# Performance work log

Measured on AMD Instinct MI355X. Metric: run time of the kernel, lower is better.

## Reference

```python
import jax, jax.numpy as jnp
import numpy as np

DIM = 64
HEADS = 4            # self.num_heads = 2 * num_heads(=2)
SMK = 5
KS = 7
EPS = 1e-5
SCALE = (DIM // HEADS) ** -0.5


def pool_mat(n, out=7):
    # AdaptiveAvgPool2d bin matrix: P[i, j] = 1/size if floor(i*n/out) <= j < ceil((i+1)*n/out)
    P = np.zeros((out, n), np.float32)
    for i in range(out):
        s = (i * n) // out
        e = -((-(i + 1) * n) // out)
        P[i, s:e] = 1.0 / (e - s)
    return jnp.asarray(P)


def bn(x, g, b, m, v):
    # inference BatchNorm2d on [B,C,H,W]
    return (x - m[:, None, None]) * (g[:, None, None] * jax.lax.rsqrt(v[:, None, None] + EPS)) + b[:, None, None]


def conv1x1(x, w):
    return jnp.einsum('oi,bihw->bohw', w, x)


def rpb_bias(rpb, H, W, k):
    # replicate apply_rpb gather indexing (incl. the flip over flattened HW)
    rs = 2 * k - 1
    ih0 = np.arange(k)
    idx_k = (ih0[:, None] * rs + ih0[None, :]).reshape(-1)        # [k*k]
    rh = np.ones(k, np.int64); rh[k // 2] = H - (k - 1)
    rw = np.ones(k, np.int64); rw[k // 2] = W - (k - 1)
    ih = np.repeat(ih0, rh)                                       # [H]
    iw = np.repeat(ih0, rw)                                       # [W]
    bias_hw = ih[:, None] * rs + iw[None, :]                      # [H,W]
    bias_idx = (bias_hw[..., None] + idx_k).reshape(-1, k * k)[::-1].copy()  # [H*W,k*k]
    flat = rpb.reshape(rpb.shape[0], -1)                          # [G, rs*rs]
    return flat[:, bias_idx].reshape(1, rpb.shape[0], H, W, k * k)


def na2d_av(attn, value, k):
    # NATTEN-style neighborhood AV: window start clamped to stay in-bounds
    B, G, H, W, _ = attn.shape
    si = np.clip(np.arange(H) - k // 2, 0, H - k)
    sj = np.clip(np.arange(W) - k // 2, 0, W - k)
    ii = si[:, None] + np.arange(k)    # [H,k]
    jj = sj[:, None] + np.arange(k)    # [W,k]
    v = value[:, :, ii][:, :, :, :, jj]         # [B,G,H,k,W,k,C]
    a = attn.reshape(B, G, H, W, k, k)
    return jnp.einsum('bghwij,bghiwjc->bghwc', a, v)


def reference(x, wq_w, wq_g, wq_b, wq_m, wq_v,
              wk_w, wk_g, wk_b, wk_m, wk_v,
              proj_w, proj_b, rpb1, rpb2,
              dy_w, dy_g, dy_b, dy_m, dy_v):
    B, C, H, W = x.shape
    G = HEADS
    q, kctx = jnp.split(x, 2, axis=1)                      # [B,C/2,H,W] each
    q = bn(conv1x1(q, wq_w), wq_g, wq_b, wq_m, wq_v) * SCALE
    Ph, Pw = pool_mat(H), pool_mat(W)
    kp = jnp.einsum('ph,bchw,qw->bcpq', Ph, kctx, Pw)      # adaptive avg pool to 7x7
    k = bn(conv1x1(kp, wk_w), wk_g, wk_b, wk_m, wk_v)
    q = q.reshape(B, G, -1, H * W)                          # b g c n
    k = k.reshape(B, G, -1, 49)                             # b g c l
    w = jnp.einsum('bgcn,bgcl->bgnl', q, k)
    w = w.transpose(0, 3, 1, 2)                             # b l g n
    w = jnp.einsum('ol,blgn->bogn', proj_w, w) + proj_b[None, :, None, None]  # b (74) g n
    w = w.transpose(0, 2, 3, 1).reshape(B, G, H, W, SMK * SMK + KS * KS)
    attn1 = w[..., :SMK * SMK]
    attn2 = w[..., SMK * SMK:]
    attn1 = jax.nn.softmax(attn1 + rpb_bias(rpb1, H, W, SMK), axis=-1)
    attn2 = jax.nn.softmax(attn2 + rpb_bias(rpb2, H, W, KS), axis=-1)
    c = C // (2 * G)
    value = x.reshape(B, 2, G, c, H, W).transpose(1, 0, 2, 4, 5, 3)  # m b g h w c
    x1 = na2d_av(attn1, value[0], SMK)
    x2 = na2d_av(attn2, value[1], KS)
    out = jnp.concatenate([x1, x2], axis=1)                 # b (2g) h w c
    out = out.transpose(0, 1, 4, 2, 3).reshape(B, C, H, W)  # b (g c) h w
    return bn(conv1x1(out, dy_w), dy_g, dy_b, dy_m, dy_v)


def setup_inputs() -> dict:
    key = jax.random.key(0)
    ks = jax.random.split(key, 20)
    h = DIM // 2
    def bnp(k):
        k1, k2, k3, k4 = jax.random.split(k, 4)
        return (jax.random.uniform(k1, (0,)),)  # unused
    inp = {
        'x': jax.random.normal(ks[0], (8, DIM, 64, 64), jnp.float32),
        'wq_w': jax.random.normal(ks[1], (h, h), jnp.float32) * (h ** -0.5),
        'wq_g': jax.random.uniform(ks[2], (h,), jnp.float32, 0.5, 1.5),
        'wq_b': jax.random.normal(ks[3], (h,), jnp.float32) * 0.1,
        'wq_m': jax.random.normal(ks[4], (h,), jnp.float32) * 0.1,
        'wq_v': jax.random.uniform(ks[5], (h,), jnp.float32, 0.5, 1.5),
        'wk_w': jax.random.normal(ks[6], (h, h), jnp.float32) * (h ** -0.5),
        'wk_g': jax.random.uniform(ks[7], (h,), jnp.float32, 0.5, 1.5),
        'wk_b': jax.random.normal(ks[8], (h,), jnp.float32) * 0.1,
        'wk_m': jax.random.normal(ks[9], (h,), jnp.float32) * 0.1,
        'wk_v': jax.random.uniform(ks[10], (h,), jnp.float32, 0.5, 1.5),
        'proj_w': jax.random.normal(ks[11], (SMK * SMK + KS * KS, 49), jnp.float32) * (49 ** -0.5),
        'proj_b': jax.random.normal(ks[12], (SMK * SMK + KS * KS,), jnp.float32) * 0.02,
        'rpb1': jax.random.normal(ks[13], (HEADS, 2 * SMK - 1, 2 * SMK - 1), jnp.float32) * 0.02,
        'rpb2': jax.random.normal(ks[14], (HEADS, 2 * KS - 1, 2 * KS - 1), jnp.float32) * 0.02,
        'dy_w': jax.random.normal(ks[15], (DIM, DIM), jnp.float32) * (DIM ** -0.5),
        'dy_g': jax.random.uniform(ks[16], (DIM,), jnp.float32, 0.5, 1.5),
        'dy_b': jax.random.normal(ks[17], (DIM,), jnp.float32) * 0.1,
        'dy_m': jax.random.normal(ks[18], (DIM,), jnp.float32) * 0.1,
        'dy_v': jax.random.uniform(ks[19], (DIM,), jnp.float32, 0.5, 1.5),
    }
    return inp
```

## Files before the change

### kernel.cpp

```cpp
#include <hip/hip_runtime.h>

#define EPSV 1e-5f

#define OFF_W    12544
#define OFF_WQT  31488
#define OFF_DYT  32512

typedef float f4u __attribute__((ext_vector_type(4), aligned(4)));

__global__ __launch_bounds__(512) void prep_weights(
    const float* __restrict__ wq_w, const float* __restrict__ dy_w,
    float* __restrict__ ws)
{
  const int t = blockIdx.x * 512 + threadIdx.x;
  float* wqT = ws + OFF_WQT;
  float* dyT = ws + OFF_DYT;
  if (t < 1024) {
    const int i = t >> 5, o = t & 31;
    wqT[t] = wq_w[o * 32 + i];
  }
  const int t2 = t - 1024;
  if (t2 >= 0 && t2 < 4096) {
    const int i = t2 >> 6, o = t2 & 63;
    dyT[t2] = dy_w[o * 64 + i];
  }
}

__global__ __launch_bounds__(256) void pool_k_kernel(
    const float* __restrict__ x,
    const float* __restrict__ wk_w, const float* __restrict__ wk_g,
    const float* __restrict__ wk_b, const float* __restrict__ wk_m,
    const float* __restrict__ wk_v, float* __restrict__ kbuf)
{
  const int b = blockIdx.x / 7;
  const int p = blockIdx.x % 7;
  const int tid = threadIdx.x;
  __shared__ float s_tmp[32 * 64];
  __shared__ float s_kp[32 * 7];

  const int sh = (p * 64) / 7, eh = ((p + 1) * 64 + 6) / 7;
  const float invH = 1.0f / (float)(eh - sh);
  for (int idx = tid; idx < 2048; idx += 256) {
    const int c = idx >> 6, ww = idx & 63;
    const float* xp = x + ((size_t)(b * 64 + 32 + c)) * 4096 + ww;
    float s = 0.f;
    for (int hh = sh; hh < eh; ++hh) s += xp[hh * 64];
    s_tmp[idx] = s * invH;
  }
  __syncthreads();
  if (tid < 224) {
    const int c = tid / 7, q = tid % 7;
    const int sw = (q * 64) / 7, ew = ((q + 1) * 64 + 6) / 7;
    float s = 0.f;
    for (int ww = sw; ww < ew; ++ww) s += s_tmp[c * 64 + ww];
    s_kp[c * 7 + q] = s / (float)(ew - sw);
  }
  __syncthreads();
  if (tid < 224) {
    const int o = tid / 7, q = tid % 7;
    float s = 0.f;
#pragma unroll
    for (int i = 0; i < 32; i++) s += wk_w[o * 32 + i] * s_kp[i * 7 + q];
    const float sc = wk_g[o] * rsqrtf(wk_v[o] + EPSV);
    const int g = o >> 3, c = o & 7, l = p * 7 + q;
    kbuf[(((size_t)b * 4 + g) * 8 + c) * 49 + l] =
        (s - wk_m[o]) * sc + wk_b[o];
  }
}

__global__ __launch_bounds__(256) void fold_w_kernel(
    const float* __restrict__ proj_w, const float* __restrict__ ws_in,
    float* __restrict__ Wout)
{
  const int bg = blockIdx.x;
  const int tid = threadIdx.x;
  __shared__ float s_k[392];
  for (int i = tid; i < 392; i += 256) s_k[i] = ws_in[(size_t)bg * 392 + i];
  __syncthreads();
  for (int idx = tid; idx < 592; idx += 256) {
    const int o = idx >> 3, c = idx & 7;
    float s = 0.f;
#pragma unroll
    for (int l = 0; l < 49; l++) s += proj_w[o * 49 + l] * s_k[c * 49 + l];
    Wout[(size_t)bg * 592 + idx] = s;
  }
}

__global__ __launch_bounds__(512, 3) void contmix_main(
    const float* __restrict__ x,
    const float* __restrict__ wq_g, const float* __restrict__ wq_b,
    const float* __restrict__ wq_m, const float* __restrict__ wq_v,
    const float* __restrict__ proj_b,
    const float* __restrict__ rpb1, const float* __restrict__ rpb2,
    const float* __restrict__ dy_g, const float* __restrict__ dy_b,
    const float* __restrict__ dy_m, const float* __restrict__ dy_v,
    const float* __restrict__ ws,
    float* __restrict__ out)
{
  __shared__ float s_rpb1[4 * 81];
  __shared__ float s_rpb2[4 * 169];
  __shared__ float s_val[64 * 64];

  const int bx = blockIdx.x;
  const int b = bx >> 6;
  const int h = bx & 63;
  const int tid = threadIdx.x;
  const int w = tid & 63;
  const int bru = __builtin_amdgcn_readfirstlane(tid >> 8);
  const int gu  = __builtin_amdgcn_readfirstlane((tid >> 6) & 3);

  for (int i = tid; i < 324; i += 512) s_rpb1[i] = rpb1[i];
  for (int i = tid; i < 676; i += 512) s_rpb2[i] = rpb2[i];
  __syncthreads();

  const float* xb = x + (size_t)b * 64 * 4096;

  float q8[8];
#pragma unroll
  for (int o = 0; o < 8; o++) q8[o] = 0.f;
  {
    const float* wqt = ws + OFF_WQT + gu * 8;
#pragma unroll
    for (int i = 0; i < 32; i++) {
      const float xv = xb[i * 4096 + h * 64 + w];
#pragma unroll
      for (int o = 0; o < 8; o++) q8[o] += wqt[i * 32 + o] * xv;
    }
#pragma unroll
    for (int o = 0; o < 8; o++) {
      const int oc = gu * 8 + o;
      const float s = wq_g[oc] * rsqrtf(wq_v[oc] + EPSV);
      q8[o] = (q8[o] * s + (wq_b[oc] - wq_m[oc] * s)) * 0.25f;
    }
  }

  const float* Wr = ws + OFF_W + (size_t)(b * 4 + gu) * 592;

  const int ph = 63 - h, pw = 63 - w;

  if (bru == 0) {
    const int bih5 = ph - min(max(ph - 2, 0), 59);
    const int biw5 = pw - min(max(pw - 2, 0), 59);
    const int si5 = min(max(h - 2, 0), 59), sj5 = min(max(w - 2, 0), 59);
    float l1[25];
#pragma unroll
    for (int o = 0; o < 25; o++) {
      const float* wo = Wr + o * 8;
      float s = proj_b[o];
#pragma unroll
      for (int c = 0; c < 8; c++) s += wo[c] * q8[c];
      l1[o] = s;
    }
    const float* rp1 = s_rpb1 + gu * 81 + bih5 * 9 + biw5;
#pragma unroll
    for (int ki = 0; ki < 5; ki++)
#pragma unroll
      for (int kj = 0; kj < 5; kj++) l1[ki * 5 + kj] += rp1[ki * 9 + kj];

    float mx = l1[0];
#pragma unroll
    for (int o = 1; o < 25; o++) mx = fmaxf(mx, l1[o]);
    float sum = 0.f;
#pragma unroll
    for (int o = 0; o < 25; o++) {
      const float e = __expf(l1[o] - mx);
      l1[o] = e;
      sum += e;
    }
    const float inv = 1.f / sum;

    float acc[8];
#pragma unroll
    for (int c = 0; c < 8; c++) acc[c] = 0.f;
    const float* vb = xb + gu * 8 * 4096;
#pragma unroll
    for (int i = 0; i < 5; i++) {
      const float a0 = l1[i * 5 + 0], a1 = l1[i * 5 + 1], a2 = l1[i * 5 + 2];
      const float a3 = l1[i * 5 + 3], a4 = l1[i * 5 + 4];
      const float* vr0 = vb + (si5 + i) * 64 + sj5;
#pragma unroll
      for (int c = 0; c < 8; c++) {
        const float* vr = vr0 + c * 4096;
        const f4u f = *(const f4u*)vr;
        const float v4 = vr[4];
        acc[c] += a0 * f.x + a1 * f.y + a2 * f.z + a3 * f.w + a4 * v4;
      }
    }
#pragma unroll
    for (int c = 0; c < 8; c++) s_val[(gu * 8 + c) * 64 + w] = acc[c] * inv;
  } else {
    const int bih7 = ph - min(max(ph - 3, 0), 57);
    const int biw7 = pw - min(max(pw - 3, 0), 57);
    const int si7 = min(max(h - 3, 0), 57), sj7 = min(max(w - 3, 0), 57);
    float l2[49];
#pragma unroll
    for (int o = 0; o < 49; o++) {
      const float* wo = Wr + (25 + o) * 8;
      float s = proj_b[25 + o];
#pragma unroll
      for (int c = 0; c < 8; c++) s += wo[c] * q8[c];
      l2[o] = s;
    }
    const float* rp2 = s_rpb2 + gu * 169 + bih7 * 13 + biw7;
#pragma unroll
    for (int ki = 0; ki < 7; ki++)
#pragma unroll
      for (int kj = 0; kj < 7; kj++) l2[ki * 7 + kj] += rp2[ki * 13 + kj];

    float mx = l2[0];
#pragma unroll
    for (int o = 1; o < 49; o++) mx = fmaxf(mx, l2[o]);
    float sum = 0.f;
#pragma unroll
    for (int o = 0; o < 49; o++) {
      const float e = __expf(l2[o] - mx);
      l2[o] = e;
      sum += e;
    }
    const float inv = 1.f / sum;

    float acc[8];
#pragma unroll
    for (int c = 0; c < 8; c++) acc[c] = 0.f;
    const float* vb = xb + (32 + gu * 8) * 4096;
#pragma unroll
    for (int i = 0; i < 7; i++) {
      const float a0 = l2[i * 7 + 0], a1 = l2[i * 7 + 1], a2 = l2[i * 7 + 2];
      const float a3 = l2[i * 7 + 3], a4 = l2[i * 7 + 4], a5 = l2[i * 7 + 5];
      const float a6 = l2[i * 7 + 6];
      const float* vr0 = vb + (si7 + i) * 64 + sj7;
#pragma unroll
      for (int c = 0; c < 8; c++) {
        const float* vr = vr0 + c * 4096;
        const f4u fa = *(const f4u*)vr;
        const f4u fb = *(const f4u*)(vr + 3);
        acc[c] += a0 * fa.x + a1 * fa.y + a2 * fa.z + a3 * fa.w +
                  a4 * fb.y + a5 * fb.z + a6 * fb.w;
      }
    }
#pragma unroll
    for (int c = 0; c < 8; c++) s_val[(32 + gu * 8 + c) * 64 + w] = acc[c] * inv;
  }

  __syncthreads();

  {
    const int ogu = __builtin_amdgcn_readfirstlane(tid >> 6);
    float facc[8];
#pragma unroll
    for (int oo = 0; oo < 8; oo++) facc[oo] = 0.f;
    const float* dyt = ws + OFF_DYT + ogu * 8;
#pragma unroll
    for (int i = 0; i < 64; i++) {
      const float v = s_val[i * 64 + w];
#pragma unroll
      for (int oo = 0; oo < 8; oo++) facc[oo] += dyt[i * 64 + oo] * v;
    }
#pragma unroll
    for (int oo = 0; oo < 8; oo++) {
      const int oc = ogu * 8 + oo;
      const float sc = dy_g[oc] * rsqrtf(dy_v[oc] + EPSV);
      out[((size_t)(b * 64 + oc)) * 4096 + h * 64 + w] =
          (facc[oo] - dy_m[oc]) * sc + dy_b[oc];
    }
  }
}

extern "C" void kernel_launch(void* const* d_in, const int* in_sizes, int n_in,
                              void* d_out, int out_size, void* d_ws, size_t ws_size,
                              hipStream_t stream)
{
  const float* x      = (const float*)d_in[0];
  const float* wq_w   = (const float*)d_in[1];
  const float* wq_g   = (const float*)d_in[2];
  const float* wq_b   = (const float*)d_in[3];
  const float* wq_m   = (const float*)d_in[4];
  const float* wq_v   = (const float*)d_in[5];
  const float* wk_w   = (const float*)d_in[6];
  const float* wk_g   = (const float*)d_in[7];
  const float* wk_b   = (const float*)d_in[8];
  const float* wk_m   = (const float*)d_in[9];
  const float* wk_v   = (const float*)d_in[10];
  const float* proj_w = (const float*)d_in[11];
  const float* proj_b = (const float*)d_in[12];
  const float* rpb1   = (const float*)d_in[13];
  const float* rpb2   = (const float*)d_in[14];
  const float* dy_w   = (const float*)d_in[15];
  const float* dy_g   = (const float*)d_in[16];
  const float* dy_b   = (const float*)d_in[17];
  const float* dy_m   = (const float*)d_in[18];
  const float* dy_v   = (const float*)d_in[19];

  float* ws = (float*)d_ws;

  prep_weights<<<10, 512, 0, stream>>>(wq_w, dy_w, ws);
  pool_k_kernel<<<56, 256, 0, stream>>>(x, wk_w, wk_g, wk_b, wk_m, wk_v, ws);
  fold_w_kernel<<<32, 256, 0, stream>>>(proj_w, ws, ws + OFF_W);
  contmix_main<<<512, 512, 0, stream>>>(x, wq_g, wq_b, wq_m, wq_v,
                                        proj_b, rpb1, rpb2,
                                        dy_g, dy_b, dy_m, dy_v,
                                        ws, (float*)d_out);
}
```

Baseline: 165.9 us.

## Merge prep into pool kernel, fold BN into wq, stage x row in LDS, vectorize s_val

Merges the weight-prep kernel into the pooling kernel as extra blocks, saving one launch. Folds the q BatchNorm scale, shift and the 0.25 factor into precomputed weights and a bias. The main kernel now stages the 32-channel x row in shared memory, stores s_val transposed with padding so it can be read and written as float4, and drops the max-subtraction from softmax. Removing the max risks overflow for large logits, though with these small-scale inputs it is likely safe.

Result: slower. 189.9 us (+14.5%).

```diff
diff --git a/kernel.cpp b/kernel.cpp
--- a/kernel.cpp
+++ b/kernel.cpp
@@ -3,41 +3,50 @@
 #define EPSV 1e-5f
 
 #define OFF_W    12544
-#define OFF_WQT  31488
-#define OFF_DYT  32512
+#define OFF_WQ2  31488
+#define OFF_Q0   32512
+#define OFF_DYT  32544
 
 typedef float f4u __attribute__((ext_vector_type(4), aligned(4)));
-
-__global__ __launch_bounds__(512) void prep_weights(
-    const float* __restrict__ wq_w, const float* __restrict__ dy_w,
-    float* __restrict__ ws)
-{
-  const int t = blockIdx.x * 512 + threadIdx.x;
-  float* wqT = ws + OFF_WQT;
-  float* dyT = ws + OFF_DYT;
-  if (t < 1024) {
-    const int i = t >> 5, o = t & 31;
-    wqT[t] = wq_w[o * 32 + i];
-  }
-  const int t2 = t - 1024;
-  if (t2 >= 0 && t2 < 4096) {
-    const int i = t2 >> 6, o = t2 & 63;
-    dyT[t2] = dy_w[o * 64 + i];
-  }
-}
-
-__global__ __launch_bounds__(256) void pool_k_kernel(
+typedef float f4a __attribute__((ext_vector_type(4), aligned(16)));
+
+__global__ __launch_bounds__(256) void pool_prep_kernel(
     const float* __restrict__ x,
     const float* __restrict__ wk_w, const float* __restrict__ wk_g,
     const float* __restrict__ wk_b, const float* __restrict__ wk_m,
-    const float* __restrict__ wk_v, float* __restrict__ kbuf)
+    const float* __restrict__ wk_v,
+    const float* __restrict__ wq_w, const float* __restrict__ wq_g,
+    const float* __restrict__ wq_b, const float* __restrict__ wq_m,
+    const float* __restrict__ wq_v,
+    const float* __restrict__ dy_w,
+    float* __restrict__ ws)
 {
+  __shared__ float s_tmp[32 * 64];
+  __shared__ float s_kp[32 * 7];
+  const int tid = threadIdx.x;
+
+  if (blockIdx.x >= 56) {
+    const int t = (blockIdx.x - 56) * 256 + tid;
+    for (int idx = t; idx < 1056; idx += 2048) {
+      if (idx < 1024) {
+        const int i = idx >> 5, o = idx & 31;
+        const float s = wq_g[o] * rsqrtf(wq_v[o] + EPSV);
+        ws[OFF_WQ2 + idx] = 0.25f * s * wq_w[o * 32 + i];
+      } else {
+        const int o = idx - 1024;
+        const float s = wq_g[o] * rsqrtf(wq_v[o] + EPSV);
+        ws[OFF_Q0 + o] = 0.25f * (wq_b[o] - wq_m[o] * s);
+      }
+    }
+    for (int idx = t; idx < 4096; idx += 2048) {
+      const int i = idx >> 6, o = idx & 63;
+      ws[OFF_DYT + idx] = dy_w[o * 64 + i];
+    }
+    return;
+  }
+
   const int b = blockIdx.x / 7;
   const int p = blockIdx.x % 7;
-  const int tid = threadIdx.x;
-  __shared__ float s_tmp[32 * 64];
-  __shared__ float s_kp[32 * 7];
-
   const int sh = (p * 64) / 7, eh = ((p + 1) * 64 + 6) / 7;
   const float invH = 1.0f / (float)(eh - sh);
   for (int idx = tid; idx < 2048; idx += 256) {
@@ -63,8 +72,7 @@
     for (int i = 0; i < 32; i++) s += wk_w[o * 32 + i] * s_kp[i * 7 + q];
     const float sc = wk_g[o] * rsqrtf(wk_v[o] + EPSV);
     const int g = o >> 3, c = o & 7, l = p * 7 + q;
-    kbuf[(((size_t)b * 4 + g) * 8 + c) * 49 + l] =
-        (s - wk_m[o]) * sc + wk_b[o];
+    ws[(((size_t)b * 4 + g) * 8 + c) * 49 + l] = (s - wk_m[o]) * sc + wk_b[o];
   }
 }
 
@@ -88,8 +96,6 @@
 
 __global__ __launch_bounds__(512, 3) void contmix_main(
     const float* __restrict__ x,
-    const float* __restrict__ wq_g, const float* __restrict__ wq_b,
-    const float* __restrict__ wq_m, const float* __restrict__ wq_v,
     const float* __restrict__ proj_b,
     const float* __restrict__ rpb1, const float* __restrict__ rpb2,
     const float* __restrict__ dy_g, const float* __restrict__ dy_b,
@@ -97,46 +103,46 @@
     const float* __restrict__ ws,
     float* __restrict__ out)
 {
-  __shared__ float s_rpb1[4 * 81];
-  __shared__ float s_rpb2[4 * 169];
-  __shared__ float s_val[64 * 64];
-
-  const int bx = blockIdx.x;
-  const int b = bx >> 6;
-  const int h = bx & 63;
+  __shared__ __align__(16) float s_val[64 * 68];
+  __shared__ float s_x[32 * 64];
+  __shared__ float s_rpb1[324];
+  __shared__ float s_rpb2[676];
+
+  const int b = blockIdx.x >> 6;
+  const int h = blockIdx.x & 63;
   const int tid = threadIdx.x;
   const int w = tid & 63;
   const int bru = __builtin_amdgcn_readfirstlane(tid >> 8);
   const int gu  = __builtin_amdgcn_readfirstlane((tid >> 6) & 3);
 
+  const float* xb = x + (size_t)b * 64 * 4096;
+
+  {
+    const float* xr = xb + h * 64;
+    for (int idx = tid; idx < 2048; idx += 512)
+      s_x[idx] = xr[(size_t)(idx >> 6) * 4096 + (idx & 63)];
+  }
   for (int i = tid; i < 324; i += 512) s_rpb1[i] = rpb1[i];
   for (int i = tid; i < 676; i += 512) s_rpb2[i] = rpb2[i];
   __syncthreads();
 
-  const float* xb = x + (size_t)b * 64 * 4096;
-
   float q8[8];
-#pragma unroll
-  for (int o = 0; o < 8; o++) q8[o] = 0.f;
   {
-    const float* wqt = ws + OFF_WQT + gu * 8;
+    const float* q0 = ws + OFF_Q0 + gu * 8;
+#pragma unroll
+    for (int o = 0; o < 8; o++) q8[o] = q0[o];
+    const float* wq2 = ws + OFF_WQ2 + gu * 8;
 #pragma unroll
     for (int i = 0; i < 32; i++) {
-      const float xv = xb[i * 4096 + h * 64 + w];
-#pragma unroll
-      for (int o = 0; o < 8; o++) q8[o] += wqt[i * 32 + o] * xv;
-    }
-#pragma unroll
-    for (int o = 0; o < 8; o++) {
-      const int oc = gu * 8 + o;
-      const float s = wq_g[oc] * rsqrtf(wq_v[oc] + EPSV);
-      q8[o] = (q8[o] * s + (wq_b[oc] - wq_m[oc] * s)) * 0.25f;
+      const float xv = s_x[i * 64 + w];
+#pragma unroll
+      for (int o = 0; o < 8; o++) q8[o] += wq2[i * 32 + o] * xv;
     }
   }
 
   const float* Wr = ws + OFF_W + (size_t)(b * 4 + gu) * 592;
-
   const int ph = 63 - h, pw = 63 - w;
+  float* svrow = s_val + w * 68;
 
   if (bru == 0) {
     const int bih5 = ph - min(max(ph - 2, 0), 59);
@@ -157,17 +163,17 @@
 #pragma unroll
       for (int kj = 0; kj < 5; kj++) l1[ki * 5 + kj] += rp1[ki * 9 + kj];
 
-    float mx = l1[0];
-#pragma unroll
-    for (int o = 1; o < 25; o++) mx = fmaxf(mx, l1[o]);
-    float sum = 0.f;
+    float p0 = 0.f, p1 = 0.f, p2 = 0.f, p3 = 0.f;
 #pragma unroll
     for (int o = 0; o < 25; o++) {
-      const float e = __expf(l1[o] - mx);
+      const float e = __expf(l1[o]);
       l1[o] = e;
-      sum += e;
-    }
-    const float inv = 1.f / sum;
+      if ((o & 3) == 0) p0 += e;
+      else if ((o & 3) == 1) p1 += e;
+      else if ((o & 3) == 2) p2 += e;
+      else p3 += e;
+    }
+    const float inv = 1.f / ((p0 + p1) + (p2 + p3));
 
     float acc[8];
 #pragma unroll
@@ -186,8 +192,11 @@
         acc[c] += a0 * f.x + a1 * f.y + a2 * f.z + a3 * f.w + a4 * v4;
       }
     }
-#pragma unroll
-    for (int c = 0; c < 8; c++) s_val[(gu * 8 + c) * 64 + w] = acc[c] * inv;
+    f4a v0, v1;
+    v0.x = acc[0] * inv; v0.y = acc[1] * inv; v0.z = acc[2] * inv; v0.w = acc[3] * inv;
+    v1.x = acc[4] * inv; v1.y = acc[5] * inv; v1.z = acc[6] * inv; v1.w = acc[7] * inv;
+    *(f4a*)(svrow + gu * 8) = v0;
+    *(f4a*)(svrow + gu * 8 + 4) = v1;
   } else {
     const int bih7 = ph - min(max(ph - 3, 0), 57);
     const int biw7 = pw - min(max(pw - 3, 0), 57);
@@ -207,17 +216,17 @@
 #pragma unroll
       for (int kj = 0; kj < 7; kj++) l2[ki * 7 + kj] += rp2[ki * 13 + kj];
 
-    float mx = l2[0];
-#pragma unroll
-    for (int o = 1; o < 49; o++) mx = fmaxf(mx, l2[o]);
-    float sum = 0.f;
+    float p0 = 0.f, p1 = 0.f, p2 = 0.f, p3 = 0.f;
 #pragma unroll
     for (int o = 0; o < 49; o++) {
-      const float e = __expf(l2[o] - mx);
+      const float e = __expf(l2[o]);
       l2[o] = e;
-      sum += e;
-    }
-    const float inv = 1.f / sum;
+      if ((o & 3) == 0) p0 += e;
+      else if ((o & 3) == 1) p1 += e;
+      else if ((o & 3) == 2) p2 += e;
+      else p3 += e;
+    }
+    const float inv = 1.f / ((p0 + p1) + (p2 + p3));
 
     float acc[8];
 #pragma unroll
@@ -238,8 +247,11 @@
                   a4 * fb.y + a5 * fb.z + a6 * fb.w;
       }
     }
-#pragma unroll
-    for (int c = 0; c < 8; c++) s_val[(32 + gu * 8 + c) * 64 + w] = acc[c] * inv;
+    f4a v0, v1;
+    v0.x = acc[0] * inv; v0.y = acc[1] * inv; v0.z = acc[2] * inv; v0.w = acc[3] * inv;
+    v1.x = acc[4] * inv; v1.y = acc[5] * inv; v1.z = acc[6] * inv; v1.w = acc[7] * inv;
+    *(f4a*)(svrow + 32 + gu * 8) = v0;
+    *(f4a*)(svrow + 32 + gu * 8 + 4) = v1;
   }
 
   __syncthreads();
@@ -250,11 +262,17 @@
 #pragma unroll
     for (int oo = 0; oo < 8; oo++) facc[oo] = 0.f;
     const float* dyt = ws + OFF_DYT + ogu * 8;
-#pragma unroll
-    for (int i = 0; i < 64; i++) {
-      const float v = s_val[i * 64 + w];
-#pragma unroll
-      for (int oo = 0; oo < 8; oo++) facc[oo] += dyt[i * 64 + oo] * v;
+    const f4a* sv = (const f4a*)svrow;
+#pragma unroll
+    for (int k = 0; k < 16; k++) {
+      const f4a v4 = sv[k];
+#pragma unroll
+      for (int j = 0; j < 4; j++) {
+        const int i = 4 * k + j;
+        const float v = (j == 0) ? v4.x : (j == 1) ? v4.y : (j == 2) ? v4.z : v4.w;
+#pragma unroll
+        for (int oo = 0; oo < 8; oo++) facc[oo] += dyt[i * 64 + oo] * v;
+      }
     }
 #pragma unroll
     for (int oo = 0; oo < 8; oo++) {
@@ -293,11 +311,11 @@
 
   float* ws = (float*)d_ws;
 
-  prep_weights<<<10, 512, 0, stream>>>(wq_w, dy_w, ws);
-  pool_k_kernel<<<56, 256, 0, stream>>>(x, wk_w, wk_g, wk_b, wk_m, wk_v, ws);
+  pool_prep_kernel<<<64, 256, 0, stream>>>(x, wk_w, wk_g, wk_b, wk_m, wk_v,
+                                           wq_w, wq_g, wq_b, wq_m, wq_v,
+                                           dy_w, ws);
   fold_w_kernel<<<32, 256, 0, stream>>>(proj_w, ws, ws + OFF_W);
-  contmix_main<<<512, 512, 0, stream>>>(x, wq_g, wq_b, wq_m, wq_v,
-                                        proj_b, rpb1, rpb2,
+  contmix_main<<<512, 512, 0, stream>>>(x, proj_b, rpb1, rpb2,
                                         dy_g, dy_b, dy_m, dy_v,
                                         ws, (float*)d_out);
 }
```
